# Performance work log

Measured on AMD Instinct MI355X. Metric: run time of the kernel, lower is better.

Reference implementation:

```python
import jax, jax.numpy as jnp
import numpy as np

B, F, K, DEPTH = 512, 64, 64, 3  # feas == k == 64, deepDepth == 3


def setup_inputs() -> dict:
    key = jax.random.key(0)
    ks = jax.random.split(key, 16)
    x = jax.random.normal(ks[0], (B, F), dtype=jnp.float32)
    # wide: Linear(feas, 1)
    Ww = jax.random.normal(ks[1], (1, F), dtype=jnp.float32) * 0.1
    bw = jnp.zeros((1,), dtype=jnp.float32)
    # cross: Parameter(torch.rand(feas, k))
    cross = jax.random.uniform(ks[2], (F, K), dtype=jnp.float32)
    # attention: Linear(k, k) -> ReLU -> Linear(k, 1, bias=False)
    W1 = jax.random.normal(ks[3], (K, K), dtype=jnp.float32) / np.sqrt(K)
    b1 = jnp.zeros((K,), dtype=jnp.float32)
    w2 = jax.random.normal(ks[4], (K,), dtype=jnp.float32) / np.sqrt(K)
    # deep{i}: Linear(k//i, k//(i+1)) + ReLU, i = 1..DEPTH  -> 64->32->21->16
    dims = [K // i for i in range(1, DEPTH + 2)]  # [64, 32, 21, 16]
    Wd1 = jax.random.normal(ks[5], (dims[1], dims[0]), dtype=jnp.float32) / np.sqrt(dims[0])
    bd1 = jnp.zeros((dims[1],), dtype=jnp.float32)
    Wd2 = jax.random.normal(ks[6], (dims[2], dims[1]), dtype=jnp.float32) / np.sqrt(dims[1])
    bd2 = jnp.zeros((dims[2],), dtype=jnp.float32)
    Wd3 = jax.random.normal(ks[7], (dims[3], dims[2]), dtype=jnp.float32) / np.sqrt(dims[2])
    bd3 = jnp.zeros((dims[3],), dtype=jnp.float32)
    # out: Linear(feas // (deepDepth+1), 1) == Linear(16, 1)
    Wo = jax.random.normal(ks[8], (1, F // (DEPTH + 1)), dtype=jnp.float32) * 0.1
    bo = jnp.zeros((1,), dtype=jnp.float32)
    return {"x": x, "Ww": Ww, "bw": bw, "cross": cross, "W1": W1, "b1": b1,
            "w2": w2, "Wd1": Wd1, "bd1": bd1, "Wd2": Wd2, "bd2": bd2,
            "Wd3": Wd3, "bd3": bd3, "Wo": Wo, "bo": bo}


def reference(x, Ww, bw, cross, W1, b1, w2, Wd1, bd1, Wd2, bd2, Wd3, bd3, Wo, bo):
    linear = x @ Ww.T + bw  # [B, 1]

    # Pairwise FM interactions v[b,i,j,:] = x_i * x_j * (cross_i ∘ cross_j)
    xx = x[:, :, None] * x[:, None, :]                    # [B, F, F]
    cp = cross[:, None, :] * cross[None, :, :]            # [F, F, K]
    v = xx[..., None] * cp[None]                          # [B, F, F, K]

    # attention MLP score per pair
    h = jax.nn.relu(jnp.einsum('bijk,lk->bijl', v, W1) + b1)
    s = jnp.einsum('bijl,l->bij', h, w2)                  # [B, F, F]

    # loop semantics: upper triangle (j >= i), pair kept iff x_i != 0 and x_j != 0
    valid = jnp.triu(jnp.ones((F, F), dtype=bool))[None] \
        & (x[:, :, None] != 0) & (x[:, None, :] != 0)     # [B, F, F]
    neg = jnp.finfo(s.dtype).min
    logits = jnp.where(valid, s, neg)

    # softmax over [0 (seed zeros(1) entry), valid pair scores...];
    # the seed zeros(k) value-vector contributes nothing to the weighted sum.
    m = jnp.maximum(jnp.max(logits, axis=(1, 2)), 0.0)    # [B]
    e = jnp.where(valid, jnp.exp(logits - m[:, None, None]), 0.0)
    denom = jnp.exp(-m) + jnp.sum(e, axis=(1, 2))         # +exp(-m) is the 0-logit term
    tmp = jnp.einsum('bij,bijk->bk', e, v) / denom[:, None]  # [B, K]

    tmp = jax.nn.relu(tmp @ Wd1.T + bd1)
    tmp = jax.nn.relu(tmp @ Wd2.T + bd2)
    tmp = jax.nn.relu(tmp @ Wd3.T + bd3)
    deep_out = tmp @ Wo.T + bo                            # [B, 1]
    return jax.nn.sigmoid(linear + deep_out)
```

## Files before the change

kernel.cpp:

```cpp
#include <hip/hip_runtime.h>
#include <math.h>


#define BB 512
#define FF 64
#define STR 68
#define NPAIRS 2080
#define THREADS 512
#define NEG_BIG -3.402823466e38f

typedef _Float16 half8 __attribute__((ext_vector_type(8)));
typedef _Float16 half4 __attribute__((ext_vector_type(4)));
typedef float f32x4 __attribute__((ext_vector_type(4)));

__device__ __forceinline__ half8 ld8(const _Float16* p) {
    half8 v;
    *(half4*)&v       = *(const half4*)p;
    *((half4*)&v + 1) = *(const half4*)(p + 4);
    return v;
}

__global__ __launch_bounds__(THREADS, 4) void afm_r7_kernel(
    const float* __restrict__ x,
    const float* __restrict__ Ww,
    const float* __restrict__ bw,
    const float* __restrict__ cross,
    const float* __restrict__ W1,
    const float* __restrict__ b1,
    const float* __restrict__ w2,
    const float* __restrict__ Wd1,
    const float* __restrict__ bd1,
    const float* __restrict__ Wd2,
    const float* __restrict__ bd2,
    const float* __restrict__ Wd3,
    const float* __restrict__ bd3,
    const float* __restrict__ Wo,
    const float* __restrict__ bo,
    float* __restrict__ out)
{
    __shared__ __align__(16) _Float16 ah_s [FF * STR];
    __shared__ __align__(16) _Float16 aht_s[FF * STR];
    __shared__ __align__(16) _Float16 M_s  [FF * STR];
    __shared__ float s_s[NPAIRS];
    __shared__ unsigned short lut_s[NPAIRS];
    __shared__ float x_sh[FF];
    __shared__ float part_s[4][FF];
    __shared__ float mlp_s[FF];
    __shared__ float red_s[16];

    const int tid  = threadIdx.x;
    const int lane = tid & 63;
    const int wave = tid >> 6;
    const int b    = blockIdx.x;
    const int m    = lane & 15;
    const int q    = lane >> 4;

    if (tid < FF) x_sh[tid] = x[b * FF + tid];
    __syncthreads();

    for (int idx = tid; idx < FF * FF; idx += THREADS) {
        const int i = idx >> 6, k = idx & 63;
        const _Float16 v = (_Float16)(x_sh[i] * cross[idx]);
        ah_s[i * STR + k]  = v;
        aht_s[k * STR + i] = v;
    }
    for (int idx = tid; idx < (FF * STR) / 2; idx += THREADS)
        ((int*)M_s)[idx] = 0;
    for (int p = tid; p < NPAIRS; p += THREADS) {
        int i = (int)floorf((129.0f - sqrtf(16641.0f - 8.0f * (float)p)) * 0.5f);
        int base = (i * (129 - i)) >> 1;
        if (p < base) { --i; base = (i * (129 - i)) >> 1; }
        else { const int nb = ((i + 1) * (128 - i)) >> 1; if (p >= nb) { ++i; base = nb; } }
        const int j = i + (p - base);
        const int valid = ((x_sh[i] != 0.f) && (x_sh[j] != 0.f)) ? 0x8000 : 0;
        lut_s[p] = (unsigned short)((i << 8) | j | valid);
    }

    half8 afr[4][2];
    #pragma unroll
    for (int mt = 0; mt < 4; ++mt)
        #pragma unroll
        for (int kt = 0; kt < 2; ++kt) {
            const float* wr = W1 + (mt * 16 + m) * FF + kt * 32 + q * 8;
            const f32x4 w0 = *(const f32x4*)wr;
            const f32x4 w1 = *(const f32x4*)(wr + 4);
            half8 h;
            #pragma unroll
            for (int jj = 0; jj < 4; ++jj) {
                h[jj]     = (_Float16)w0[jj];
                h[4 + jj] = (_Float16)w1[jj];
            }
            afr[mt][kt] = h;
        }
    float b1r[16], w2r[16];
    #pragma unroll
    for (int mt = 0; mt < 4; ++mt) {
        const f32x4 bb = *(const f32x4*)(b1 + mt * 16 + q * 4);
        const f32x4 ww = *(const f32x4*)(w2 + mt * 16 + q * 4);
        #pragma unroll
        for (int r = 0; r < 4; ++r) {
            b1r[mt * 4 + r] = bb[r];
            w2r[mt * 4 + r] = ww[r];
        }
    }
    __syncthreads();

    float wave_mx = 0.0f;
    for (int i = wave; i < FF; i += 8) {
        const half8 sA0 = ld8(&ah_s[i * STR + q * 8]);
        const half8 sA1 = ld8(&ah_s[i * STR + 32 + q * 8]);
        const bool  xi_nz = (x_sh[i] != 0.f);
        const int   base_i = (i * (129 - i)) >> 1;
        for (int jt = (i >> 4); jt < 4; ++jt) {
            const int j = jt * 16 + m;
            const half8 B0 = sA0 * ld8(&ah_s[j * STR + q * 8]);
            const half8 B1 = sA1 * ld8(&ah_s[j * STR + 32 + q * 8]);
            float sp = 0.f;
            #pragma unroll
            for (int mt = 0; mt < 4; ++mt) {
                f32x4 acc;
                #pragma unroll
                for (int r = 0; r < 4; ++r) acc[r] = b1r[mt * 4 + r];
                acc = __builtin_amdgcn_mfma_f32_16x16x32_f16(afr[mt][0], B0, acc, 0, 0, 0);
                acc = __builtin_amdgcn_mfma_f32_16x16x32_f16(afr[mt][1], B1, acc, 0, 0, 0);
                #pragma unroll
                for (int r = 0; r < 4; ++r)
                    sp = fmaf(w2r[mt * 4 + r], fmaxf(acc[r], 0.f), sp);
            }
            sp += __shfl_xor(sp, 16, 64);
            sp += __shfl_xor(sp, 32, 64);
            const bool cover = (j >= i) && xi_nz && (x_sh[j] != 0.f);
            wave_mx = fmaxf(wave_mx, cover ? sp : 0.f);
            if (lane < 16 && j >= i)
                s_s[base_i + (j - i)] = sp;
        }
    }
    wave_mx = fmaxf(wave_mx, __shfl_xor(wave_mx, 1, 64));
    wave_mx = fmaxf(wave_mx, __shfl_xor(wave_mx, 2, 64));
    wave_mx = fmaxf(wave_mx, __shfl_xor(wave_mx, 4, 64));
    wave_mx = fmaxf(wave_mx, __shfl_xor(wave_mx, 8, 64));
    if (lane == 0) red_s[wave] = wave_mx;
    __syncthreads();

    float mval = red_s[0];
    #pragma unroll
    for (int w = 1; w < 8; ++w) mval = fmaxf(mval, red_s[w]);

    float sum = 0.f;
    for (int p = tid; p < NPAIRS; p += THREADS) {
        const int ij = lut_s[p];
        const float e = (ij & 0x8000) ? __expf(s_s[p] - mval) : 0.f;
        sum += e;
        M_s[((ij >> 8) & 63) * STR + (ij & 63)] = (_Float16)e;
    }
    #pragma unroll
    for (int off = 32; off > 0; off >>= 1)
        sum += __shfl_xor(sum, off, 64);
    if (lane == 0) red_s[8 + wave] = sum;
    __syncthreads();
    float denom = __expf(-mval);
    #pragma unroll
    for (int w = 0; w < 8; ++w) denom += red_s[8 + w];

    {
        const int t0 = wave * 2;
        #pragma unroll
        for (int t = t0; t < t0 + 2; ++t) {
            const int i0 = (t >> 2) * 16, k0 = (t & 3) * 16;
            const half8 a0  = ld8(&M_s[(i0 + m) * STR + q * 8]);
            const half8 a1  = ld8(&M_s[(i0 + m) * STR + 32 + q * 8]);
            const half8 bb0 = ld8(&aht_s[(k0 + m) * STR + q * 8]);
            const half8 bb1 = ld8(&aht_s[(k0 + m) * STR + 32 + q * 8]);
            f32x4 g = {0.f, 0.f, 0.f, 0.f};
            g = __builtin_amdgcn_mfma_f32_16x16x32_f16(a0, bb0, g, 0, 0, 0);
            g = __builtin_amdgcn_mfma_f32_16x16x32_f16(a1, bb1, g, 0, 0, 0);
            const half4 ap = *(const half4*)&aht_s[(k0 + m) * STR + i0 + q * 4];
            float s4 = (float)ap[0] * g[0] + (float)ap[1] * g[1]
                     + (float)ap[2] * g[2] + (float)ap[3] * g[3];
            s4 += __shfl_xor(s4, 16, 64);
            s4 += __shfl_xor(s4, 32, 64);
            if (lane < 16) part_s[i0 >> 4][k0 + lane] = s4;
        }
    }
    __syncthreads();
    if (tid < FF)
        mlp_s[tid] = (part_s[0][tid] + part_s[1][tid] +
                      part_s[2][tid] + part_s[3][tid]) / denom;
    __syncthreads();

    float* tmp2 = part_s[0];

    {
        const int outi = tid >> 4, kp = tid & 15;
        float a = 0.f;
        #pragma unroll
        for (int t = 0; t < 4; ++t)
            a = fmaf(Wd1[outi * 64 + kp + t * 16], mlp_s[kp + t * 16], a);
        a += __shfl_xor(a, 1, 64);
        a += __shfl_xor(a, 2, 64);
        a += __shfl_xor(a, 4, 64);
        a += __shfl_xor(a, 8, 64);
        if (kp == 0) tmp2[outi] = fmaxf(a + bd1[outi], 0.f);
    }
    __syncthreads();

    if (tid < 21 * 8) {
        const int outi = tid >> 3, kp = tid & 7;
        float a = 0.f;
        #pragma unroll
        for (int t = 0; t < 4; ++t)
            a = fmaf(Wd2[outi * 32 + kp + t * 8], tmp2[kp + t * 8], a);
        a += __shfl_xor(a, 1, 64);
        a += __shfl_xor(a, 2, 64);
        a += __shfl_xor(a, 4, 64);
        if (kp == 0) mlp_s[outi] = fmaxf(a + bd2[outi], 0.f);
    }
    __syncthreads();

    if (tid < 16 * 8) {
        const int outi = tid >> 3, kp = tid & 7;
        float a = Wd3[outi * 21 + kp] * mlp_s[kp];
        a = fmaf(Wd3[outi * 21 + kp + 8], mlp_s[kp + 8], a);
        if (kp < 5) a = fmaf(Wd3[outi * 21 + kp + 16], mlp_s[kp + 16], a);
        a += __shfl_xor(a, 1, 64);
        a += __shfl_xor(a, 2, 64);
        a += __shfl_xor(a, 4, 64);
        if (kp == 0) tmp2[outi] = fmaxf(a + bd3[outi], 0.f);
    }
    __syncthreads();

    if (wave == 0) {
        float v = Ww[lane] * x_sh[lane];
        if (lane < 16) v = fmaf(Wo[lane], tmp2[lane], v);
        #pragma unroll
        for (int off = 32; off > 0; off >>= 1)
            v += __shfl_xor(v, off, 64);
        if (lane == 0) {
            const float z = v + bw[0] + bo[0];
            out[b] = 1.f / (1.f + __expf(-z));
        }
    }
}

extern "C" void kernel_launch(void* const* d_in, const int* in_sizes, int n_in,
                              void* d_out, int out_size, void* d_ws, size_t ws_size,
                              hipStream_t stream) {
    const float* xp    = (const float*)d_in[0];
    const float* Ww    = (const float*)d_in[1];
    const float* bw    = (const float*)d_in[2];
    const float* cross = (const float*)d_in[3];
    const float* W1    = (const float*)d_in[4];
    const float* b1    = (const float*)d_in[5];
    const float* w2    = (const float*)d_in[6];
    const float* Wd1   = (const float*)d_in[7];
    const float* bd1   = (const float*)d_in[8];
    const float* Wd2   = (const float*)d_in[9];
    const float* bd2   = (const float*)d_in[10];
    const float* Wd3   = (const float*)d_in[11];
    const float* bd3   = (const float*)d_in[12];
    const float* Wo    = (const float*)d_in[13];
    const float* bo    = (const float*)d_in[14];
    float* outp = (float*)d_out;

    afm_r7_kernel<<<BB, THREADS, 0, stream>>>(xp, Ww, bw, cross, W1, b1, w2,
                                              Wd1, bd1, Wd2, bd2, Wd3, bd3,
                                              Wo, bo, outp);
}
```

Baseline: 105.7 us.

## Fuse pair scoring, softmax and weighted sum into one pass with fixed shift

Pairs are now walked in 16-pair tiles through the index LUT, covering only the upper triangle instead of whole 16-wide j tiles. The exponentiated score and the e·v weighted sum are accumulated in registers in the same pass, which removes the score buffer, the weight matrix, the transposed copy, the second MFMA contraction and one block-wide max reduction plus its barriers. The running max is replaced by a constant shift of 20. This is exact in theory, but it relies on scores staying in a range where exp(s-20) neither overflows nor underflows badly. Staging of x*cross is vectorised, and extra barriers were added around the small MLP writes.

```diff
diff --git a/kernel.cpp b/kernel.cpp
--- a/kernel.cpp
+++ b/kernel.cpp
@@ -7,7 +7,8 @@
 #define STR 68
 #define NPAIRS 2080
 #define THREADS 512
-#define NEG_BIG -3.402823466e38f
+#define NIT 130
+#define SHIFT 20.0f
 
 typedef _Float16 half8 __attribute__((ext_vector_type(8)));
 typedef _Float16 half4 __attribute__((ext_vector_type(4)));
@@ -20,7 +21,7 @@
     return v;
 }
 
-__global__ __launch_bounds__(THREADS, 4) void afm_r7_kernel(
+__global__ __launch_bounds__(THREADS, 4) void afm_r10_kernel(
     const float* __restrict__ x,
     const float* __restrict__ Ww,
     const float* __restrict__ bw,
@@ -38,15 +39,12 @@
     const float* __restrict__ bo,
     float* __restrict__ out)
 {
-    __shared__ __align__(16) _Float16 ah_s [FF * STR];
-    __shared__ __align__(16) _Float16 aht_s[FF * STR];
-    __shared__ __align__(16) _Float16 M_s  [FF * STR];
-    __shared__ float s_s[NPAIRS];
+    __shared__ __align__(16) _Float16 ah_s[FF * STR];
     __shared__ unsigned short lut_s[NPAIRS];
     __shared__ float x_sh[FF];
-    __shared__ float part_s[4][FF];
+    __shared__ float part_s[8][FF];
+    __shared__ float red_s[8];
     __shared__ float mlp_s[FF];
-    __shared__ float red_s[16];
 
     const int tid  = threadIdx.x;
     const int lane = tid & 63;
@@ -58,14 +56,17 @@
     if (tid < FF) x_sh[tid] = x[b * FF + tid];
     __syncthreads();
 
-    for (int idx = tid; idx < FF * FF; idx += THREADS) {
-        const int i = idx >> 6, k = idx & 63;
-        const _Float16 v = (_Float16)(x_sh[i] * cross[idx]);
-        ah_s[i * STR + k]  = v;
-        aht_s[k * STR + i] = v;
-    }
-    for (int idx = tid; idx < (FF * STR) / 2; idx += THREADS)
-        ((int*)M_s)[idx] = 0;
+    #pragma unroll
+    for (int t = 0; t < 2; ++t) {
+        const int idx4 = (tid + t * THREADS) * 4;
+        const int i = idx4 >> 6, k = idx4 & 63;
+        const f32x4 c4 = *(const f32x4*)(cross + idx4);
+        const float xi = x_sh[i];
+        half4 h;
+        #pragma unroll
+        for (int jj = 0; jj < 4; ++jj) h[jj] = (_Float16)(xi * c4[jj]);
+        *(half4*)&ah_s[i * STR + k] = h;
+    }
     for (int p = tid; p < NPAIRS; p += THREADS) {
         int i = (int)floorf((129.0f - sqrtf(16641.0f - 8.0f * (float)p)) * 0.5f);
         int base = (i * (129 - i)) >> 1;
@@ -105,87 +106,73 @@
     }
     __syncthreads();
 
-    float wave_mx = 0.0f;
-    for (int i = wave; i < FF; i += 8) {
-        const half8 sA0 = ld8(&ah_s[i * STR + q * 8]);
-        const half8 sA1 = ld8(&ah_s[i * STR + 32 + q * 8]);
-        const bool  xi_nz = (x_sh[i] != 0.f);
-        const int   base_i = (i * (129 - i)) >> 1;
-        for (int jt = (i >> 4); jt < 4; ++jt) {
-            const int j = jt * 16 + m;
-            const half8 B0 = sA0 * ld8(&ah_s[j * STR + q * 8]);
-            const half8 B1 = sA1 * ld8(&ah_s[j * STR + 32 + q * 8]);
-            float sp = 0.f;
+    float acc[16];
+    #pragma unroll
+    for (int jj = 0; jj < 16; ++jj) acc[jj] = 0.f;
+    float d = 0.f;
+
+    int lutw = lut_s[wave * 16 + m];
+    for (int it = wave; it < NIT; it += 8) {
+        const int ij = lutw;
+        const int i = (ij >> 8) & 63, j = ij & 63;
+        const half8 r0 = ld8(&ah_s[i * STR + q * 8]);
+        const half8 s0 = ld8(&ah_s[j * STR + q * 8]);
+        const half8 r1 = ld8(&ah_s[i * STR + 32 + q * 8]);
+        const half8 s1 = ld8(&ah_s[j * STR + 32 + q * 8]);
+        if (it + 8 < NIT) lutw = lut_s[(it + 8) * 16 + m];
+        const half8 b0 = r0 * s0;
+        const half8 b1v = r1 * s1;
+        float pp[4];
+        #pragma unroll
+        for (int mt = 0; mt < 4; ++mt) {
+            f32x4 a;
             #pragma unroll
-            for (int mt = 0; mt < 4; ++mt) {
-                f32x4 acc;
-                #pragma unroll
-                for (int r = 0; r < 4; ++r) acc[r] = b1r[mt * 4 + r];
-                acc = __builtin_amdgcn_mfma_f32_16x16x32_f16(afr[mt][0], B0, acc, 0, 0, 0);
-                acc = __builtin_amdgcn_mfma_f32_16x16x32_f16(afr[mt][1], B1, acc, 0, 0, 0);
-                #pragma unroll
-                for (int r = 0; r < 4; ++r)
-                    sp = fmaf(w2r[mt * 4 + r], fmaxf(acc[r], 0.f), sp);
-            }
-            sp += __shfl_xor(sp, 16, 64);
-            sp += __shfl_xor(sp, 32, 64);
-            const bool cover = (j >= i) && xi_nz && (x_sh[j] != 0.f);
-            wave_mx = fmaxf(wave_mx, cover ? sp : 0.f);
-            if (lane < 16 && j >= i)
-                s_s[base_i + (j - i)] = sp;
-        }
-    }
-    wave_mx = fmaxf(wave_mx, __shfl_xor(wave_mx, 1, 64));
-    wave_mx = fmaxf(wave_mx, __shfl_xor(wave_mx, 2, 64));
-    wave_mx = fmaxf(wave_mx, __shfl_xor(wave_mx, 4, 64));
-    wave_mx = fmaxf(wave_mx, __shfl_xor(wave_mx, 8, 64));
-    if (lane == 0) red_s[wave] = wave_mx;
-    __syncthreads();
-
-    float mval = red_s[0];
-    #pragma unroll
-    for (int w = 1; w < 8; ++w) mval = fmaxf(mval, red_s[w]);
-
-    float sum = 0.f;
-    for (int p = tid; p < NPAIRS; p += THREADS) {
-        const int ij = lut_s[p];
-        const float e = (ij & 0x8000) ? __expf(s_s[p] - mval) : 0.f;
-        sum += e;
-        M_s[((ij >> 8) & 63) * STR + (ij & 63)] = (_Float16)e;
-    }
-    #pragma unroll
-    for (int off = 32; off > 0; off >>= 1)
-        sum += __shfl_xor(sum, off, 64);
-    if (lane == 0) red_s[8 + wave] = sum;
-    __syncthreads();
-    float denom = __expf(-mval);
-    #pragma unroll
-    for (int w = 0; w < 8; ++w) denom += red_s[8 + w];
-
-    {
-        const int t0 = wave * 2;
-        #pragma unroll
-        for (int t = t0; t < t0 + 2; ++t) {
-            const int i0 = (t >> 2) * 16, k0 = (t & 3) * 16;
-            const half8 a0  = ld8(&M_s[(i0 + m) * STR + q * 8]);
-            const half8 a1  = ld8(&M_s[(i0 + m) * STR + 32 + q * 8]);
-            const half8 bb0 = ld8(&aht_s[(k0 + m) * STR + q * 8]);
-            const half8 bb1 = ld8(&aht_s[(k0 + m) * STR + 32 + q * 8]);
-            f32x4 g = {0.f, 0.f, 0.f, 0.f};
-            g = __builtin_amdgcn_mfma_f32_16x16x32_f16(a0, bb0, g, 0, 0, 0);
-            g = __builtin_amdgcn_mfma_f32_16x16x32_f16(a1, bb1, g, 0, 0, 0);
-            const half4 ap = *(const half4*)&aht_s[(k0 + m) * STR + i0 + q * 4];
-            float s4 = (float)ap[0] * g[0] + (float)ap[1] * g[1]
-                     + (float)ap[2] * g[2] + (float)ap[3] * g[3];
-            s4 += __shfl_xor(s4, 16, 64);
-            s4 += __shfl_xor(s4, 32, 64);
-            if (lane < 16) part_s[i0 >> 4][k0 + lane] = s4;
-        }
-    }
-    __syncthreads();
-    if (tid < FF)
-        mlp_s[tid] = (part_s[0][tid] + part_s[1][tid] +
-                      part_s[2][tid] + part_s[3][tid]) / denom;
+            for (int r = 0; r < 4; ++r) a[r] = b1r[mt * 4 + r];
+            a = __builtin_amdgcn_mfma_f32_16x16x32_f16(afr[mt][0], b0,  a, 0, 0, 0);
+            a = __builtin_amdgcn_mfma_f32_16x16x32_f16(afr[mt][1], b1v, a, 0, 0, 0);
+            float s = 0.f;
+            #pragma unroll
+            for (int r = 0; r < 4; ++r)
+                s = fmaf(w2r[mt * 4 + r], fmaxf(a[r], 0.f), s);
+            pp[mt] = s;
+        }
+        float sp = (pp[0] + pp[1]) + (pp[2] + pp[3]);
+        sp += __shfl_xor(sp, 16, 64);
+        sp += __shfl_xor(sp, 32, 64);
+        const float e = (ij & 0x8000) ? __expf(sp - SHIFT) : 0.f;
+        d += e;
+        #pragma unroll
+        for (int jj = 0; jj < 8; ++jj) {
+            acc[jj]     = fmaf(e, (float)b0[jj],  acc[jj]);
+            acc[8 + jj] = fmaf(e, (float)b1v[jj], acc[8 + jj]);
+        }
+    }
+
+    #pragma unroll
+    for (int off = 1; off <= 8; off <<= 1) {
+        d += __shfl_xor(d, off, 64);
+        #pragma unroll
+        for (int jj = 0; jj < 16; ++jj)
+            acc[jj] += __shfl_xor(acc[jj], off, 64);
+    }
+    if (m == 0) {
+        #pragma unroll
+        for (int jj = 0; jj < 8; ++jj) {
+            part_s[wave][q * 8 + jj]      = acc[jj];
+            part_s[wave][32 + q * 8 + jj] = acc[8 + jj];
+        }
+        if (lane == 0) red_s[wave] = d;
+    }
+    __syncthreads();
+
+    if (tid < FF) {
+        const float dd = ((red_s[0] + red_s[1]) + (red_s[2] + red_s[3]))
+                       + ((red_s[4] + red_s[5]) + (red_s[6] + red_s[7]));
+        const float denom = __expf(-SHIFT) + dd;
+        const float t = ((part_s[0][tid] + part_s[1][tid]) + (part_s[2][tid] + part_s[3][tid]))
+                      + ((part_s[4][tid] + part_s[5][tid]) + (part_s[6][tid] + part_s[7][tid]));
+        mlp_s[tid] = t / denom;
+    }
     __syncthreads();
 
     float* tmp2 = part_s[0];
@@ -204,6 +191,7 @@
     }
     __syncthreads();
 
+    float hv = 0.f;
     if (tid < 21 * 8) {
         const int outi = tid >> 3, kp = tid & 7;
         float a = 0.f;
@@ -213,8 +201,10 @@
         a += __shfl_xor(a, 1, 64);
         a += __shfl_xor(a, 2, 64);
         a += __shfl_xor(a, 4, 64);
-        if (kp == 0) mlp_s[outi] = fmaxf(a + bd2[outi], 0.f);
-    }
+        hv = fmaxf(a + bd2[outi], 0.f);
+    }
+    __syncthreads();
+    if (tid < 21 * 8 && (tid & 7) == 0) mlp_s[tid >> 3] = hv;
     __syncthreads();
 
     if (tid < 16 * 8) {
@@ -225,8 +215,10 @@
         a += __shfl_xor(a, 1, 64);
         a += __shfl_xor(a, 2, 64);
         a += __shfl_xor(a, 4, 64);
-        if (kp == 0) tmp2[outi] = fmaxf(a + bd3[outi], 0.f);
-    }
+        hv = fmaxf(a + bd3[outi], 0.f);
+    }
+    __syncthreads();
+    if (tid < 16 * 8 && (tid & 7) == 0) tmp2[tid >> 3] = hv;
     __syncthreads();
 
     if (wave == 0) {
@@ -262,7 +254,7 @@
     const float* bo    = (const float*)d_in[14];
     float* outp = (float*)d_out;
 
-    afm_r7_kernel<<<BB, THREADS, 0, stream>>>(xp, Ww, bw, cross, W1, b1, w2,
-                                              Wd1, bd1, Wd2, bd2, Wd3, bd3,
-                                              Wo, bo, outp);
+    afm_r10_kernel<<<BB, THREADS, 0, stream>>>(xp, Ww, bw, cross, W1, b1, w2,
+                                               Wd1, bd1, Wd2, bd2, Wd3, bd3,
+                                               Wo, bo, outp);
 }
```

New measurement: 106.4 us. About the same (+0.7%).
